# Optimization experiments

Measured on AMD Instinct MI355X. Metric: run time of the kernel, lower is better.

Reference implementation:

```python
import jax, jax.numpy as jnp
import numpy as np

COMMITMENT_BETA = 0.25


def setup_inputs() -> dict:
    key = jax.random.key(0)
    k1, k2 = jax.random.split(key)
    B, D, H, W = 32, 256, 32, 32
    NUM_CODES = 1024
    z = jax.random.normal(k1, (B, D, H, W), dtype=jnp.float32)
    codebook = jax.random.normal(k2, (NUM_CODES, D), dtype=jnp.float32)
    return {"z": z, "codebook": codebook}


def reference(z, codebook):
    # z: [B, D, H, W], codebook: [K, D]
    B, D, H, W = z.shape
    z_flat = jnp.transpose(z, (0, 2, 3, 1)).reshape(-1, D)  # [N, D]
    # squared euclidean distances: ||z||^2 - 2 z.W^T + ||W||^2  -> [N, K]
    d = (
        jnp.sum(z_flat * z_flat, axis=1, keepdims=True)
        - 2.0 * (z_flat @ codebook.T)
        + jnp.sum(codebook * codebook, axis=1)[None, :]
    )
    indices = jnp.argmin(d, axis=1)  # [N]
    z_q_flat = codebook[indices]  # [N, D] gather
    # commitment loss: mse(z_flat, stop_grad(z_q_flat))
    diff = z_flat - jax.lax.stop_gradient(z_q_flat)
    commitment_loss = jnp.mean(diff * diff)
    # straight-through estimator
    z_q_flat = z_flat + jax.lax.stop_gradient(z_q_flat - z_flat)
    z_q = jnp.transpose(z_q_flat.reshape(B, H, W, D), (0, 3, 1, 2))
    indices = indices.reshape(B, H, W)
    return z_q, indices, COMMITMENT_BETA * commitment_loss
```

## Files before the change

kernel.cpp:

```cpp
#include <hip/hip_runtime.h>
#include <hip/hip_bf16.h>
#include <hip/hip_fp16.h>

#define DD  256
#define HWD 1024
#define NN  32768
#define KK  1024
#define ZQ_SIZE (NN*DD)
#define IDX_OFF ZQ_SIZE
#define LOSS_OFF (ZQ_SIZE + NN)

#define CBH_OFF    0
#define CNORM_OFF  (KK*DD*2)
#define ZSQ_OFF    (CNORM_OFF + KK*4)
#define ROWREC_OFF (ZSQ_OFF + 2048)

#define TH_REFINE 0.2f
#define LOSS_SCALE (0.25f / (float)ZQ_SIZE)

typedef __attribute__((ext_vector_type(8))) _Float16 h16x8;
typedef __attribute__((ext_vector_type(4))) float f32x4;

__device__ __forceinline__ void gload16(const void* g, void* l) {
    __builtin_amdgcn_global_load_lds(
        (const __attribute__((address_space(1))) void*)g,
        (__attribute__((address_space(3))) void*)l, 16, 0, 0);
}
__device__ __forceinline__ short f16bits(float x) {
    _Float16 h = (_Float16)x;
    return *reinterpret_cast<short*>(&h);
}

__global__ __launch_bounds__(256)
void vq_prep_kernel(const float* __restrict__ cb, unsigned char* __restrict__ scratch) {
    _Float16* cbh = (_Float16*)(scratch + CBH_OFF);
    float* cn = (float*)(scratch + CNORM_OFF);
    int t = threadIdx.x;
    int row = blockIdx.x * 16 + (t >> 4);
    int dq  = t & 15;
    const float* rp = cb + (size_t)row * DD + dq * 16;
    float nrm = 0.f;
    __attribute__((aligned(16))) _Float16 h[16];
#pragma unroll
    for (int i = 0; i < 4; ++i) {
        float4 v = *(const float4*)(rp + i * 4);
        float xs[4] = {v.x, v.y, v.z, v.w};
#pragma unroll
        for (int j = 0; j < 4; ++j) {
            float x = xs[j];
            h[i * 4 + j] = (_Float16)x;
            nrm = fmaf(x, x, nrm);
        }
    }
    *(uint4*)&cbh[(size_t)row * DD + dq * 16]     = *(uint4*)&h[0];
    *(uint4*)&cbh[(size_t)row * DD + dq * 16 + 8] = *(uint4*)&h[8];
#pragma unroll
    for (int m = 1; m < 16; m <<= 1) nrm += __shfl_xor(nrm, m, 64);
    if (dq == 0) cn[row] = nrm;
}

__global__ __launch_bounds__(256) __attribute__((amdgpu_waves_per_eu(2, 2)))
void vq_mfma_argmin_kernel(const float* __restrict__ z, unsigned char* __restrict__ scratch) {
    const unsigned char* cbh_b = scratch + CBH_OFF;
    const float* cn_g = (const float*)(scratch + CNORM_OFF);
    float* zsqp = (float*)(scratch + ZSQ_OFF);
    float* rowrec = (float*)(scratch + ROWREC_OFF);

    __shared__ __attribute__((aligned(16))) short bufs[4 * 8192];
    __shared__ float cn_l[KK];
    __shared__ float zred[4];

    const int t    = threadIdx.x;
    const int w    = t >> 6;
    const int lane = t & 63;
    const int ln15 = lane & 15;
    const int lh   = lane >> 4;
    const int g     = w >> 1;
    const int khalf = w & 1;

    const int n0  = blockIdx.x * 64;
    const int b   = n0 >> 10;
    const int hw0 = n0 & 1023;

    const int ksub  = lane >> 5;
    const int chunk = lane & 31;

    const int klr   = khalf * 16 + ln15;
    const int rbase = klr * 256;
    const int rxor  = (klr & 7) << 3;

    *(float4*)&cn_l[t * 4] = *(const float4*)(cn_g + t * 4);

    {
        short* zlds = bufs;
        const int zd = t >> 4;
        const int zq = t & 15;
        const float* zb = z + (size_t)b * DD * HWD + hw0 + zq * 4;
        float zsq = 0.f;
#pragma unroll
        for (int p = 0; p < 16; ++p) {
            int d = p * 16 + zd;
            float4 v = *(const float4*)(zb + (size_t)d * HWD);
            zsq = fmaf(v.x, v.x, zsq); zsq = fmaf(v.y, v.y, zsq);
            zsq = fmaf(v.z, v.z, zsq); zsq = fmaf(v.w, v.w, zsq);
            float xs[4] = {v.x, v.y, v.z, v.w};
#pragma unroll
            for (int i = 0; i < 4; ++i) {
                int row = zq * 4 + i;
                zlds[row * 256 + (d ^ ((row & 15) << 3))] = f16bits(xs[i]);
            }
        }
#pragma unroll
        for (int m = 1; m < 64; m <<= 1) zsq += __shfl_xor(zsq, m, 64);
        if (lane == 0) zred[w] = zsq;
    }
    __syncthreads();

    h16x8 ah[2][8];
#pragma unroll
    for (int nf = 0; nf < 2; ++nf) {
#pragma unroll
        for (int ds = 0; ds < 8; ++ds) {
            int row = g * 32 + nf * 16 + ln15;
            int d0  = ds * 32 + lh * 8;
            ah[nf][ds] = *(const h16x8*)&bufs[row * 256 + (d0 ^ ((row & 15) << 3))];
        }
    }
    if (t == 0) zsqp[blockIdx.x] = (zred[0] + zred[1]) + (zred[2] + zred[3]);
    __syncthreads();

    auto STAGE = [&](int tt) {
#pragma unroll
        for (int si = 0; si < 4; ++si) {
            int s  = w * 4 + si;
            int kl = s * 2 + ksub;
            const unsigned char* src = cbh_b
                + (size_t)(tt * 32 + kl) * 512 + ((chunk ^ (kl & 7)) << 4);
            gload16(src, &bufs[(tt & 3) * 8192 + s * 512]);
        }
    };

    float v1[8], k1f[8], v2[8], k2f[8];
#pragma unroll
    for (int s = 0; s < 8; ++s) { v1[s] = 3e38f; v2[s] = 3e38f; k1f[s] = 0.f; k2f[s] = 0.f; }

    auto COMPUTE = [&](int kt) {
        const short* cbt = &bufs[(kt & 3) * 8192];
        const float cnv = cn_l[kt * 32 + klr];
        const float kgf = (float)(kt * 32 + klr);
        f32x4 c0 = {0.f,0.f,0.f,0.f}, c1 = c0, c2 = c0, c3 = c0;
#pragma unroll
        for (int ds = 0; ds < 8; ds += 2) {
            const int ib0 = rbase + (((ds + 0) * 32 + lh * 8) ^ rxor);
            const int ib1 = rbase + (((ds + 1) * 32 + lh * 8) ^ rxor);
            h16x8 b0 = *(const h16x8*)&cbt[ib0];
            h16x8 b1 = *(const h16x8*)&cbt[ib1];
            c0 = __builtin_amdgcn_mfma_f32_16x16x32_f16(ah[0][ds + 0], b0, c0, 0, 0, 0);
            c2 = __builtin_amdgcn_mfma_f32_16x16x32_f16(ah[1][ds + 0], b0, c2, 0, 0, 0);
            c1 = __builtin_amdgcn_mfma_f32_16x16x32_f16(ah[0][ds + 1], b1, c1, 0, 0, 0);
            c3 = __builtin_amdgcn_mfma_f32_16x16x32_f16(ah[1][ds + 1], b1, c3, 0, 0, 0);
        }
        f32x4 s0 = c0 + c1, s1 = c2 + c3;
#pragma unroll
        for (int s = 0; s < 8; ++s) {
            float a = (s < 4) ? s0[s] : s1[s - 4];
            float dist = fmaf(-2.f, a, cnv);
            bool b1c = dist < v1[s];
            bool b2c = dist < v2[s];
            v2[s]  = b1c ? v1[s]  : (b2c ? dist : v2[s]);
            k2f[s] = b1c ? k1f[s] : (b2c ? kgf  : k2f[s]);
            v1[s]  = b1c ? dist : v1[s];
            k1f[s] = b1c ? kgf  : k1f[s];
        }
    };

    STAGE(0); STAGE(1); STAGE(2);

    for (int kt = 0; kt < 29; ++kt) {
        asm volatile("s_waitcnt vmcnt(8)" ::: "memory");
        __builtin_amdgcn_sched_barrier(0);
        __builtin_amdgcn_s_barrier();
        __builtin_amdgcn_sched_barrier(0);
        STAGE(kt + 3);
        COMPUTE(kt);
    }
    asm volatile("s_waitcnt vmcnt(8)" ::: "memory");
    __builtin_amdgcn_sched_barrier(0);
    __builtin_amdgcn_s_barrier();
    __builtin_amdgcn_sched_barrier(0);
    COMPUTE(29);
    asm volatile("s_waitcnt vmcnt(4)" ::: "memory");
    __builtin_amdgcn_sched_barrier(0);
    __builtin_amdgcn_s_barrier();
    __builtin_amdgcn_sched_barrier(0);
    COMPUTE(30);
    asm volatile("s_waitcnt vmcnt(0)" ::: "memory");
    __builtin_amdgcn_sched_barrier(0);
    __builtin_amdgcn_s_barrier();
    __builtin_amdgcn_sched_barrier(0);
    COMPUTE(31);

    __syncthreads();
    float* redv = (float*)bufs;
    float* redk = redv + 64 * 65;
#pragma unroll
    for (int s = 0; s < 8; ++s) {
        int nf = s >> 2, r = s & 3;
        int rowb = g * 32 + nf * 16 + lh * 4 + r;
        redv[klr * 65 + rowb]        = v1[s];
        redk[klr * 65 + rowb]        = k1f[s];
        redv[(32 + klr) * 65 + rowb] = v2[s];
        redk[(32 + klr) * 65 + rowb] = k2f[s];
    }
    __syncthreads();

    const int p = t >> 6, row = t & 63;
    float w1 = 3e38f, w2 = 3e38f, w3 = 3e38f, c1e = 0.f, c2e = 0.f, c3e = 0.f;
#pragma unroll
    for (int q = 0; q < 16; ++q) {
        int i = p * 16 + q;
        float v  = redv[i * 65 + row];
        float kf = redk[i * 65 + row];
        bool lt1 = (v < w1) || (v == w1 && kf < c1e);
        bool lt2 = (v < w2) || (v == w2 && kf < c2e);
        bool lt3 = (v < w3) || (v == w3 && kf < c3e);
        w3 = lt2 ? w2 : (lt3 ? v : w3);  c3e = lt2 ? c2e : (lt3 ? kf : c3e);
        w2 = lt1 ? w1 : (lt2 ? v : w2);  c2e = lt1 ? c1e : (lt2 ? kf : c2e);
        w1 = lt1 ? v : w1;               c1e = lt1 ? kf : c1e;
    }
    __syncthreads();
    {
        float* pv = (float*)bufs;
        float* pk = pv + 4 * 64 * 3;
        int base = (p * 64 + row) * 3;
        pv[base + 0] = w1; pk[base + 0] = c1e;
        pv[base + 1] = w2; pk[base + 1] = c2e;
        pv[base + 2] = w3; pk[base + 2] = c3e;
    }
    __syncthreads();
    if (t < 64) {
        const float* pv = (const float*)bufs;
        const float* pk = pv + 4 * 64 * 3;
        float u1 = 3e38f, u2 = 3e38f, u3 = 3e38f, d1 = 0.f, d2 = 0.f, d3 = 0.f;
#pragma unroll
        for (int i = 0; i < 12; ++i) {
            int pp = i / 3, e = i % 3;
            float v  = pv[(pp * 64 + t) * 3 + e];
            float kf = pk[(pp * 64 + t) * 3 + e];
            bool lt1 = (v < u1) || (v == u1 && kf < d1);
            bool lt2 = (v < u2) || (v == u2 && kf < d2);
            bool lt3 = (v < u3) || (v == u3 && kf < d3);
            u3 = lt2 ? u2 : (lt3 ? v : u3);  d3 = lt2 ? d2 : (lt3 ? kf : d3);
            u2 = lt1 ? u1 : (lt2 ? v : u2);  d2 = lt1 ? d1 : (lt2 ? kf : d2);
            u1 = lt1 ? v : u1;               d1 = lt1 ? kf : d1;
        }
        float4 ra; ra.x = u1; ra.y = d1; ra.z = u2; ra.w = d2;
        float4 rb; rb.x = u3; rb.y = d3; rb.z = 0.f; rb.w = 0.f;
        *(float4*)&rowrec[(size_t)(n0 + t) * 8]     = ra;
        *(float4*)&rowrec[(size_t)(n0 + t) * 8 + 4] = rb;
    }
}

__global__ __launch_bounds__(256)
void vq_refine_kernel(const float* __restrict__ z, const float* __restrict__ cb,
                      const unsigned char* __restrict__ scratch, float* __restrict__ idx_out,
                      float* __restrict__ lossp) {
    const float* rowrec = (const float*)(scratch + ROWREC_OFF);
    const float* cn_g = (const float*)(scratch + CNORM_OFF);
    const float* zsqp = (const float*)(scratch + ZSQ_OFF);
    int n = blockIdx.x * 256 + threadIdx.x;
    int lane = threadIdx.x & 63;
    float4 ra = *(const float4*)&rowrec[(size_t)n * 8];
    float4 rb = *(const float4*)&rowrec[(size_t)n * 8 + 4];
    bool flag = (ra.z - ra.x) <= TH_REFINE;
    float lp = 0.f;
    if (!flag) { idx_out[n] = ra.y; lp = ra.x; }
    unsigned long long mask = __ballot(flag);
    while (mask) {
        int li = __ffsll(mask) - 1;
        mask &= mask - 1;
        int nn  = __shfl(n, li);
        int kk1 = (int)__shfl(ra.y, li);
        int kk2 = (int)__shfl(ra.w, li);
        int kk3 = (int)__shfl(rb.y, li);
        int bb = nn >> 10, hw = nn & 1023;
        const float* zp  = z  + (size_t)bb * DD * HWD + hw;
        const float* c1p = cb + (size_t)kk1 * DD;
        const float* c2p = cb + (size_t)kk2 * DD;
        const float* c3p = cb + (size_t)kk3 * DD;
        float s1 = 0.f, s2 = 0.f, s3 = 0.f;
#pragma unroll
        for (int j = 0; j < 4; ++j) {
            int d = lane + 64 * j;
            float zv = zp[(size_t)d * HWD];
            s1 = fmaf(zv, c1p[d], s1);
            s2 = fmaf(zv, c2p[d], s2);
            s3 = fmaf(zv, c3p[d], s3);
        }
#pragma unroll
        for (int m = 32; m >= 1; m >>= 1) {
            s1 += __shfl_xor(s1, m, 64);
            s2 += __shfl_xor(s2, m, 64);
            s3 += __shfl_xor(s3, m, 64);
        }
        float e1 = cn_g[kk1] - 2.f * s1;
        float e2 = cn_g[kk2] - 2.f * s2;
        float e3 = cn_g[kk3] - 2.f * s3;
        float dch = e1; int kch = kk1;
        if (e2 < dch || (e2 == dch && kk2 < kch)) { dch = e2; kch = kk2; }
        if (e3 < dch || (e3 == dch && kk3 < kch)) { dch = e3; kch = kk3; }
        if (lane == 0) { idx_out[nn] = (float)kch; lp += dch; }
    }
    if (blockIdx.x == 0) {
        const float2 zv = *(const float2*)&zsqp[threadIdx.x * 2];
        lp += zv.x + zv.y;
    }
#pragma unroll
    for (int m = 32; m >= 1; m >>= 1) lp += __shfl_xor(lp, m, 64);
    __shared__ float bl[4];
    if (lane == 0) bl[threadIdx.x >> 6] = lp;
    __syncthreads();
    if (threadIdx.x == 0)
        atomicAdd(lossp, (bl[0] + bl[1] + bl[2] + bl[3]) * LOSS_SCALE);
}

__global__ __launch_bounds__(256)
void vq_gather_kernel(const float* __restrict__ cb, float* __restrict__ out) {
    const float* idxf = out + IDX_OFF;
    __shared__ float crow[64][257];
    __shared__ int kidx[64];
    int t = threadIdx.x;
    int w = t >> 6, lane = t & 63;
    int n0 = blockIdx.x * 64;
    int b = n0 >> 10, hw0 = n0 & 1023;
    if (t < 64) kidx[t] = (int)idxf[n0 + t];
    __syncthreads();
    for (int i = 0; i < 16; ++i) {
        int r = w * 16 + i;
        int k = kidx[r];
        float4 v = *(const float4*)(cb + (size_t)k * DD + lane * 4);
        crow[r][lane * 4 + 0] = v.x; crow[r][lane * 4 + 1] = v.y;
        crow[r][lane * 4 + 2] = v.z; crow[r][lane * 4 + 3] = v.w;
    }
    __syncthreads();
    const int zph = t >> 6, hwl = t & 63;
#pragma unroll 4
    for (int dd = 0; dd < 64; ++dd) {
        int d = dd * 4 + zph;
        size_t o = (size_t)b * (DD * HWD) + (size_t)d * HWD + hw0 + hwl;
        out[o] = crow[hwl][d];
    }
}

extern "C" void kernel_launch(void* const* d_in, const int* in_sizes, int n_in,
                              void* d_out, int out_size, void* d_ws, size_t ws_size,
                              hipStream_t stream) {
    const float* z  = (const float*)d_in[0];
    const float* cb = (const float*)d_in[1];
    float* out = (float*)d_out;
    unsigned char* scratch = (unsigned char*)d_out;

    hipMemsetAsync((void*)(out + LOSS_OFF), 0, sizeof(float), stream);

    vq_prep_kernel<<<64, 256, 0, stream>>>(cb, scratch);
    vq_mfma_argmin_kernel<<<512, 256, 0, stream>>>(z, scratch);
    vq_refine_kernel<<<128, 256, 0, stream>>>(z, cb, scratch, out + IDX_OFF, out + LOSS_OFF);
    vq_gather_kernel<<<512, 256, 0, stream>>>(cb, out);
}
```

Before: 70.15 us.

## Pack codebook index into distance mantissa bits for branchless top-k tracking

Adds a positive bias to codebook norms so distances stay positive, then overwrites the low 10 mantissa bits with the code index so a single float min/max carries both value and index. This replaces select-heavy top-2/top-3 tracking and the separate index arrays in registers, LDS and the row record with fminf/fmaxf chains, and halves the row-record size. It also changes the LDS swizzle and packs two f16 z values per 32-bit LDS store. The truncated mantissa loses precision, so the refine threshold is raised to 0.5 to send more near-ties to exact fp32 rescoring, which adds refine work.

Measured after the change: 67.93 us, median of 2. 3.2% less time.

```diff
diff --git a/kernel.cpp b/kernel.cpp
--- a/kernel.cpp
+++ b/kernel.cpp
@@ -15,7 +15,8 @@
 #define ZSQ_OFF    (CNORM_OFF + KK*4)
 #define ROWREC_OFF (ZSQ_OFF + 2048)
 
-#define TH_REFINE 0.2f
+#define DBIAS 512.0f
+#define TH_REFINE 0.5f
 #define LOSS_SCALE (0.25f / (float)ZQ_SIZE)
 
 typedef __attribute__((ext_vector_type(8))) _Float16 h16x8;
@@ -26,9 +27,12 @@
         (const __attribute__((address_space(1))) void*)g,
         (__attribute__((address_space(3))) void*)l, 16, 0, 0);
 }
-__device__ __forceinline__ short f16bits(float x) {
+__device__ __forceinline__ unsigned short f16u(float x) {
     _Float16 h = (_Float16)x;
-    return *reinterpret_cast<short*>(&h);
+    return *reinterpret_cast<unsigned short*>(&h);
+}
+__device__ __forceinline__ int swz(int row) {
+    return (row & 15) ^ ((row >> 2) & 15);
 }
 
 __global__ __launch_bounds__(256)
@@ -56,7 +60,7 @@
     *(uint4*)&cbh[(size_t)row * DD + dq * 16 + 8] = *(uint4*)&h[8];
 #pragma unroll
     for (int m = 1; m < 16; m <<= 1) nrm += __shfl_xor(nrm, m, 64);
-    if (dq == 0) cn[row] = nrm;
+    if (dq == 0) cn[row] = nrm + DBIAS;
 }
 
 __global__ __launch_bounds__(256) __attribute__((amdgpu_waves_per_eu(2, 2)))
@@ -87,7 +91,7 @@
 
     const int klr   = khalf * 16 + ln15;
     const int rbase = klr * 256;
-    const int rxor  = (klr & 7) << 3;
+    const int rxor  = swz(klr) << 3;
 
     *(float4*)&cn_l[t * 4] = *(const float4*)(cn_g + t * 4);
 
@@ -98,16 +102,22 @@
         const float* zb = z + (size_t)b * DD * HWD + hw0 + zq * 4;
         float zsq = 0.f;
 #pragma unroll
-        for (int p = 0; p < 16; ++p) {
-            int d = p * 16 + zd;
-            float4 v = *(const float4*)(zb + (size_t)d * HWD);
-            zsq = fmaf(v.x, v.x, zsq); zsq = fmaf(v.y, v.y, zsq);
-            zsq = fmaf(v.z, v.z, zsq); zsq = fmaf(v.w, v.w, zsq);
-            float xs[4] = {v.x, v.y, v.z, v.w};
+        for (int p = 0; p < 16; p += 2) {
+            int d0 = zd * 16 + p;
+            float4 va = *(const float4*)(zb + (size_t)(d0 + 0) * HWD);
+            float4 vb = *(const float4*)(zb + (size_t)(d0 + 1) * HWD);
+            zsq = fmaf(va.x, va.x, zsq); zsq = fmaf(va.y, va.y, zsq);
+            zsq = fmaf(va.z, va.z, zsq); zsq = fmaf(va.w, va.w, zsq);
+            zsq = fmaf(vb.x, vb.x, zsq); zsq = fmaf(vb.y, vb.y, zsq);
+            zsq = fmaf(vb.z, vb.z, zsq); zsq = fmaf(vb.w, vb.w, zsq);
+            float xa[4] = {va.x, va.y, va.z, va.w};
+            float xb[4] = {vb.x, vb.y, vb.z, vb.w};
 #pragma unroll
             for (int i = 0; i < 4; ++i) {
                 int row = zq * 4 + i;
-                zlds[row * 256 + (d ^ ((row & 15) << 3))] = f16bits(xs[i]);
+                int idx = row * 256 + (d0 ^ (swz(row) << 3));
+                unsigned pk = (unsigned)f16u(xa[i]) | ((unsigned)f16u(xb[i]) << 16);
+                *(unsigned*)&zlds[idx] = pk;
             }
         }
 #pragma unroll
@@ -123,7 +133,7 @@
         for (int ds = 0; ds < 8; ++ds) {
             int row = g * 32 + nf * 16 + ln15;
             int d0  = ds * 32 + lh * 8;
-            ah[nf][ds] = *(const h16x8*)&bufs[row * 256 + (d0 ^ ((row & 15) << 3))];
+            ah[nf][ds] = *(const h16x8*)&bufs[row * 256 + (d0 ^ (swz(row) << 3))];
         }
     }
     if (t == 0) zsqp[blockIdx.x] = (zred[0] + zred[1]) + (zred[2] + zred[3]);
@@ -135,19 +145,19 @@
             int s  = w * 4 + si;
             int kl = s * 2 + ksub;
             const unsigned char* src = cbh_b
-                + (size_t)(tt * 32 + kl) * 512 + ((chunk ^ (kl & 7)) << 4);
+                + (size_t)(tt * 32 + kl) * 512 + ((chunk ^ swz(kl)) << 4);
             gload16(src, &bufs[(tt & 3) * 8192 + s * 512]);
         }
     };
 
-    float v1[8], k1f[8], v2[8], k2f[8];
-#pragma unroll
-    for (int s = 0; s < 8; ++s) { v1[s] = 3e38f; v2[s] = 3e38f; k1f[s] = 0.f; k2f[s] = 0.f; }
+    float v1[8], v2[8];
+#pragma unroll
+    for (int s = 0; s < 8; ++s) { v1[s] = 3e38f; v2[s] = 3e38f; }
 
     auto COMPUTE = [&](int kt) {
         const short* cbt = &bufs[(kt & 3) * 8192];
         const float cnv = cn_l[kt * 32 + klr];
-        const float kgf = (float)(kt * 32 + klr);
+        const unsigned kbits = (unsigned)(kt * 32 + klr);
         f32x4 c0 = {0.f,0.f,0.f,0.f}, c1 = c0, c2 = c0, c3 = c0;
 #pragma unroll
         for (int ds = 0; ds < 8; ds += 2) {
@@ -165,12 +175,9 @@
         for (int s = 0; s < 8; ++s) {
             float a = (s < 4) ? s0[s] : s1[s - 4];
             float dist = fmaf(-2.f, a, cnv);
-            bool b1c = dist < v1[s];
-            bool b2c = dist < v2[s];
-            v2[s]  = b1c ? v1[s]  : (b2c ? dist : v2[s]);
-            k2f[s] = b1c ? k1f[s] : (b2c ? kgf  : k2f[s]);
-            v1[s]  = b1c ? dist : v1[s];
-            k1f[s] = b1c ? kgf  : k1f[s];
+            float pd = __uint_as_float((__float_as_uint(dist) & 0xFFFFFC00u) | kbits);
+            v2[s] = fminf(fmaxf(pd, v1[s]), v2[s]);
+            v1[s] = fminf(pd, v1[s]);
         }
     };
 
@@ -202,62 +209,43 @@
 
     __syncthreads();
     float* redv = (float*)bufs;
-    float* redk = redv + 64 * 65;
 #pragma unroll
     for (int s = 0; s < 8; ++s) {
         int nf = s >> 2, r = s & 3;
         int rowb = g * 32 + nf * 16 + lh * 4 + r;
         redv[klr * 65 + rowb]        = v1[s];
-        redk[klr * 65 + rowb]        = k1f[s];
         redv[(32 + klr) * 65 + rowb] = v2[s];
-        redk[(32 + klr) * 65 + rowb] = k2f[s];
     }
     __syncthreads();
 
     const int p = t >> 6, row = t & 63;
-    float w1 = 3e38f, w2 = 3e38f, w3 = 3e38f, c1e = 0.f, c2e = 0.f, c3e = 0.f;
+    float w1 = 3e38f, w2 = 3e38f, w3 = 3e38f;
 #pragma unroll
     for (int q = 0; q < 16; ++q) {
-        int i = p * 16 + q;
-        float v  = redv[i * 65 + row];
-        float kf = redk[i * 65 + row];
-        bool lt1 = (v < w1) || (v == w1 && kf < c1e);
-        bool lt2 = (v < w2) || (v == w2 && kf < c2e);
-        bool lt3 = (v < w3) || (v == w3 && kf < c3e);
-        w3 = lt2 ? w2 : (lt3 ? v : w3);  c3e = lt2 ? c2e : (lt3 ? kf : c3e);
-        w2 = lt1 ? w1 : (lt2 ? v : w2);  c2e = lt1 ? c1e : (lt2 ? kf : c2e);
-        w1 = lt1 ? v : w1;               c1e = lt1 ? kf : c1e;
+        float v = redv[(p * 16 + q) * 65 + row];
+        w3 = fminf(fmaxf(v, w2), w3);
+        w2 = fminf(fmaxf(v, w1), w2);
+        w1 = fminf(v, w1);
     }
     __syncthreads();
     {
         float* pv = (float*)bufs;
-        float* pk = pv + 4 * 64 * 3;
         int base = (p * 64 + row) * 3;
-        pv[base + 0] = w1; pk[base + 0] = c1e;
-        pv[base + 1] = w2; pk[base + 1] = c2e;
-        pv[base + 2] = w3; pk[base + 2] = c3e;
+        pv[base + 0] = w1; pv[base + 1] = w2; pv[base + 2] = w3;
     }
     __syncthreads();
     if (t < 64) {
         const float* pv = (const float*)bufs;
-        const float* pk = pv + 4 * 64 * 3;
-        float u1 = 3e38f, u2 = 3e38f, u3 = 3e38f, d1 = 0.f, d2 = 0.f, d3 = 0.f;
+        float u1 = 3e38f, u2 = 3e38f, u3 = 3e38f;
 #pragma unroll
         for (int i = 0; i < 12; ++i) {
-            int pp = i / 3, e = i % 3;
-            float v  = pv[(pp * 64 + t) * 3 + e];
-            float kf = pk[(pp * 64 + t) * 3 + e];
-            bool lt1 = (v < u1) || (v == u1 && kf < d1);
-            bool lt2 = (v < u2) || (v == u2 && kf < d2);
-            bool lt3 = (v < u3) || (v == u3 && kf < d3);
-            u3 = lt2 ? u2 : (lt3 ? v : u3);  d3 = lt2 ? d2 : (lt3 ? kf : d3);
-            u2 = lt1 ? u1 : (lt2 ? v : u2);  d2 = lt1 ? d1 : (lt2 ? kf : d2);
-            u1 = lt1 ? v : u1;               d1 = lt1 ? kf : d1;
-        }
-        float4 ra; ra.x = u1; ra.y = d1; ra.z = u2; ra.w = d2;
-        float4 rb; rb.x = u3; rb.y = d3; rb.z = 0.f; rb.w = 0.f;
-        *(float4*)&rowrec[(size_t)(n0 + t) * 8]     = ra;
-        *(float4*)&rowrec[(size_t)(n0 + t) * 8 + 4] = rb;
+            float v = pv[((i / 3) * 64 + t) * 3 + (i % 3)];
+            u3 = fminf(fmaxf(v, u2), u3);
+            u2 = fminf(fmaxf(v, u1), u2);
+            u1 = fminf(v, u1);
+        }
+        float4 rec; rec.x = u1; rec.y = u2; rec.z = u3; rec.w = 0.f;
+        *(float4*)&rowrec[(size_t)(n0 + t) * 4] = rec;
     }
 }
 
@@ -270,19 +258,24 @@
     const float* zsqp = (const float*)(scratch + ZSQ_OFF);
     int n = blockIdx.x * 256 + threadIdx.x;
     int lane = threadIdx.x & 63;
-    float4 ra = *(const float4*)&rowrec[(size_t)n * 8];
-    float4 rb = *(const float4*)&rowrec[(size_t)n * 8 + 4];
-    bool flag = (ra.z - ra.x) <= TH_REFINE;
+
+    float4 rr = *(const float4*)&rowrec[(size_t)n * 4];
+    unsigned b1 = __float_as_uint(rr.x);
+    bool flag = (rr.y - rr.x) <= TH_REFINE;
     float lp = 0.f;
-    if (!flag) { idx_out[n] = ra.y; lp = ra.x; }
+    if (!flag) {
+        idx_out[n] = (float)(b1 & 1023u);
+        lp = __uint_as_float(b1 & 0xFFFFFC00u) - DBIAS;
+    }
+
     unsigned long long mask = __ballot(flag);
     while (mask) {
         int li = __ffsll(mask) - 1;
         mask &= mask - 1;
         int nn  = __shfl(n, li);
-        int kk1 = (int)__shfl(ra.y, li);
-        int kk2 = (int)__shfl(ra.w, li);
-        int kk3 = (int)__shfl(rb.y, li);
+        int kk1 = (int)(__float_as_uint(__shfl(rr.x, li)) & 1023u);
+        int kk2 = (int)(__float_as_uint(__shfl(rr.y, li)) & 1023u);
+        int kk3 = (int)(__float_as_uint(__shfl(rr.z, li)) & 1023u);
         int bb = nn >> 10, hw = nn & 1023;
         const float* zp  = z  + (size_t)bb * DD * HWD + hw;
         const float* c1p = cb + (size_t)kk1 * DD;
@@ -303,14 +296,15 @@
             s2 += __shfl_xor(s2, m, 64);
             s3 += __shfl_xor(s3, m, 64);
         }
-        float e1 = cn_g[kk1] - 2.f * s1;
-        float e2 = cn_g[kk2] - 2.f * s2;
-        float e3 = cn_g[kk3] - 2.f * s3;
+        float e1 = (cn_g[kk1] - DBIAS) - 2.f * s1;
+        float e2 = (cn_g[kk2] - DBIAS) - 2.f * s2;
+        float e3 = (cn_g[kk3] - DBIAS) - 2.f * s3;
         float dch = e1; int kch = kk1;
         if (e2 < dch || (e2 == dch && kk2 < kch)) { dch = e2; kch = kk2; }
         if (e3 < dch || (e3 == dch && kk3 < kch)) { dch = e3; kch = kk3; }
         if (lane == 0) { idx_out[nn] = (float)kch; lp += dch; }
     }
+
     if (blockIdx.x == 0) {
         const float2 zv = *(const float2*)&zsqp[threadIdx.x * 2];
         lp += zv.x + zv.y;
```
